# Kernel optimization log

Hardware: AMD Instinct MI355X
Metric: run time of the kernel (lower is better)

The kernel has to match this reference:

```python
import jax, jax.numpy as jnp
import numpy as np
import math

DIM = 128
HEADS = 8
HC = DIM // HEADS  # per-head channels = 16
N = 50000
E = 800000
LEAKY_SLOPE = 0.2


def _seg_softmax(logits, seg, n):
    # numerically-stable softmax over edges grouped by destination node
    m = jax.ops.segment_max(logits, seg, num_segments=n)
    m = jnp.where(jnp.isfinite(m), m, 0.0)
    e = jnp.exp(logits - m[seg])
    s = jax.ops.segment_sum(e, seg, num_segments=n)
    return e / jnp.maximum(s[seg], 1e-16)


def setup_inputs() -> dict:
    key = jax.random.key(0)
    ks = jax.random.split(key, 20)
    sc = 1.0 / math.sqrt(DIM)
    inp = {
        "x": jax.random.normal(ks[0], (N, DIM), jnp.float32),
        "edge_index": jax.random.randint(ks[1], (2, E), 0, N, jnp.int64),
        # GATConv params
        "gat_w": jax.random.normal(ks[2], (DIM, DIM), jnp.float32) * sc,
        "gat_att_src": jax.random.normal(ks[3], (HEADS, HC), jnp.float32) * sc,
        "gat_att_dst": jax.random.normal(ks[4], (HEADS, HC), jnp.float32) * sc,
        "gat_b": jnp.zeros((DIM,), jnp.float32),
        # SAGEConv params (lin_l has bias, lin_r has none; normalize=True)
        "sage_wl": jax.random.normal(ks[5], (DIM, DIM), jnp.float32) * sc,
        "sage_bl": jnp.zeros((DIM,), jnp.float32),
        "sage_wr": jax.random.normal(ks[6], (DIM, DIM), jnp.float32) * sc,
        # TransformerConv params (q/k/v + skip, heads concat -> DIM)
        "tr_wq": jax.random.normal(ks[7], (DIM, DIM), jnp.float32) * sc,
        "tr_bq": jnp.zeros((DIM,), jnp.float32),
        "tr_wk": jax.random.normal(ks[8], (DIM, DIM), jnp.float32) * sc,
        "tr_bk": jnp.zeros((DIM,), jnp.float32),
        "tr_wv": jax.random.normal(ks[9], (DIM, DIM), jnp.float32) * sc,
        "tr_bv": jnp.zeros((DIM,), jnp.float32),
        "tr_wskip": jax.random.normal(ks[10], (DIM, DIM), jnp.float32) * sc,
        "tr_bskip": jnp.zeros((DIM,), jnp.float32),
        # fusion + layernorm
        "fus_w": jax.random.normal(ks[11], (3 * DIM, DIM), jnp.float32) * (1.0 / math.sqrt(3 * DIM)),
        "fus_b": jnp.zeros((DIM,), jnp.float32),
        "ln_g": jnp.ones((DIM,), jnp.float32),
        "ln_b": jnp.zeros((DIM,), jnp.float32),
    }
    return inp


def reference(x, edge_index, gat_w, gat_att_src, gat_att_dst, gat_b,
              sage_wl, sage_bl, sage_wr,
              tr_wq, tr_bq, tr_wk, tr_bk, tr_wv, tr_bv, tr_wskip, tr_bskip,
              fus_w, fus_b, ln_g, ln_b):
    n = x.shape[0]
    src, dst = edge_index[0], edge_index[1]  # messages flow src -> dst

    # ---- GATConv (adds self-loops, per-dst softmax attention) ----
    loop = jnp.arange(n, dtype=src.dtype)
    s2 = jnp.concatenate([src, loop])
    d2 = jnp.concatenate([dst, loop])
    h = (x @ gat_w).reshape(n, HEADS, HC)            # [N,H,C]
    a_src = (h * gat_att_src).sum(-1)                # [N,H]
    a_dst = (h * gat_att_dst).sum(-1)
    logits = jax.nn.leaky_relu(a_src[s2] + a_dst[d2], LEAKY_SLOPE)  # [E+N,H]
    alpha = _seg_softmax(logits, d2, n)
    gat_out = jax.ops.segment_sum(alpha[:, :, None] * h[s2], d2,
                                  num_segments=n).reshape(n, DIM) + gat_b

    # ---- SAGEConv (mean aggregation + root weight, L2-normalized) ----
    ones = jnp.ones(src.shape, x.dtype)
    deg = jax.ops.segment_sum(ones, dst, num_segments=n)
    nbr = jax.ops.segment_sum(x[src], dst, num_segments=n) / jnp.maximum(deg, 1.0)[:, None]
    sage_out = nbr @ sage_wl + sage_bl + x @ sage_wr
    sage_out = sage_out / jnp.maximum(
        jnp.linalg.norm(sage_out, axis=-1, keepdims=True), 1e-12)

    # ---- TransformerConv (scaled dot-product attn per dst + skip) ----
    q = (x @ tr_wq + tr_bq).reshape(n, HEADS, HC)
    k = (x @ tr_wk + tr_bk).reshape(n, HEADS, HC)
    v = (x @ tr_wv + tr_bv).reshape(n, HEADS, HC)
    t_logits = (q[dst] * k[src]).sum(-1) / math.sqrt(HC)  # [E,H]
    t_alpha = _seg_softmax(t_logits, dst, n)               # dropout off (eval)
    tr_out = jax.ops.segment_sum(t_alpha[:, :, None] * v[src], dst,
                                 num_segments=n).reshape(n, DIM)
    tr_out = tr_out + x @ tr_wskip + tr_bskip

    # ---- fusion + layernorm ----
    concat = jnp.concatenate([gat_out, sage_out, tr_out], axis=-1)
    out = concat @ fus_w + fus_b
    mu = out.mean(-1, keepdims=True)
    var = ((out - mu) ** 2).mean(-1, keepdims=True)
    return (out - mu) / jnp.sqrt(var + 1e-5) * ln_g + ln_b
```

## Files before the change

### kernel.cpp

```cpp
#include <hip/hip_runtime.h>
#include <hip/hip_bf16.h>
#include <math.h>

#define DIM 128
#define HEADS 8

typedef short short8 __attribute__((ext_vector_type(8)));
typedef float f32x4 __attribute__((ext_vector_type(4)));

#define GLD_LDS16(g, l) \
  __builtin_amdgcn_global_load_lds((const __attribute__((address_space(1))) void*)(g), \
                                   (__attribute__((address_space(3))) void*)(l), 16, 0, 0)

__device__ __forceinline__ float bf2f(unsigned short u) {
  union { unsigned int i; float f; } c; c.i = ((unsigned int)u) << 16; return c.f;
}
__device__ __forceinline__ unsigned short f2bf(float f) {
  __hip_bfloat16 h = __float2bfloat16(f);
  union { __hip_bfloat16 h; unsigned short u; } c; c.h = h; return c.u;
}
__device__ __forceinline__ float u_lo(unsigned int u) {
  union { unsigned int i; float f; } c; c.i = u << 16; return c.f;
}
__device__ __forceinline__ float u_hi(unsigned int u) {
  union { unsigned int i; float f; } c; c.i = u & 0xffff0000u; return c.f;
}

__global__ void prep_w(const float* __restrict__ gw, const float* __restrict__ wq,
                       const float* __restrict__ wk, const float* __restrict__ wv,
                       const float* __restrict__ wsk,
                       const float* __restrict__ bq, const float* __restrict__ bk,
                       const float* __restrict__ bv, const float* __restrict__ bsk,
                       const float* __restrict__ swl, const float* __restrict__ swr,
                       const float* __restrict__ fw,
                       unsigned short* __restrict__ Wcat_t, float* __restrict__ Bcat,
                       unsigned short* __restrict__ sage_t, unsigned short* __restrict__ fus_t) {
  int i = blockIdx.x * 256 + threadIdx.x;
  if (i < 81920) {
    int c = i >> 7, k = i & 127;
    int s = c >> 7, j = c & 127;
    const float* w = (s == 0) ? gw : (s == 1) ? wq : (s == 2) ? wk : (s == 3) ? wv : wsk;
    Wcat_t[i] = f2bf(w[k * 128 + j]);
  } else if (i < 114688) {
    int t = i - 81920;
    int j = t >> 8, k = t & 255;
    float v = (k < 128) ? swl[k * 128 + j] : swr[(k - 128) * 128 + j];
    sage_t[t] = f2bf(v);
  } else if (i < 163840) {
    int t = i - 114688;
    int j = t / 384, k = t - j * 384;
    fus_t[t] = f2bf(fw[k * 128 + j]);
  } else if (i < 164480) {
    int c = i - 163840;
    int s = c >> 7, j = c & 127;
    Bcat[c] = (s == 0) ? 0.f : (s == 1) ? bq[j] : (s == 2) ? bk[j] : (s == 3) ? bv[j] : bsk[j];
  }
}

__global__ void convert_x(const float* __restrict__ x, unsigned short* __restrict__ AG, int n) {
  int i = blockIdx.x * 256 + threadIdx.x;
  if (i >= n * 32) return;
  int idx = i * 4;
  float4 v = *(const float4*)(x + idx);
  ushort4 u;
  u.x = f2bf(v.x); u.y = f2bf(v.y); u.z = f2bf(v.z); u.w = f2bf(v.w);
  *(ushort4*)(AG + (size_t)(idx >> 7) * 512 + 384 + (idx & 127)) = u;
}

template <int EPI>
__global__ __launch_bounds__(256) void gemm128(
    const __hip_bfloat16* __restrict__ A0, int lda0,
    const __hip_bfloat16* __restrict__ A1, int lda1,
    const __hip_bfloat16* __restrict__ Bt, int K,
    const float* __restrict__ bias,
    unsigned short* __restrict__ AGo, float* __restrict__ Pq, float* __restrict__ Psk,
    float* __restrict__ aSo, float* __restrict__ aDo,
    const float* __restrict__ atts, const float* __restrict__ attd,
    unsigned short* __restrict__ FUSo, float* __restrict__ outF,
    const float* __restrict__ lng, const float* __restrict__ lnb,
    int M) {
  __shared__ char Asb[128 * 64];
  __shared__ char Bsb[128 * 64];
  int tid = threadIdx.x;
  int l = tid & 63, w = tid >> 6;
  int row0 = blockIdx.x * 128, col0 = blockIdx.y * 128;
  f32x4 acc[2][8] = {};

  for (int kt = 0; kt < K; kt += 32) {
    const __hip_bfloat16* Ap;
    int lda, kof;
    if (A1 != nullptr && kt >= 128) { Ap = A1; lda = lda1; kof = kt - 128; }
    else { Ap = A0; lda = lda0; kof = kt; }
#pragma unroll
    for (int it = 0; it < 2; ++it) {
      int c = it * 256 + tid;
      int r = c >> 2, cp = c & 3;
      int gp = cp ^ (r & 3);
      int gr = row0 + r; if (gr >= M) gr = M - 1;
      GLD_LDS16((const char*)(Ap + (size_t)gr * lda + kof) + gp * 16, Asb + c * 16);
    }
#pragma unroll
    for (int it = 0; it < 2; ++it) {
      int c = it * 256 + tid;
      int r = c >> 2, cp = c & 3;
      int gp = cp ^ (r & 3);
      GLD_LDS16((const char*)(Bt + (size_t)(col0 + r) * K + kt) + gp * 16, Bsb + c * 16);
    }
    __syncthreads();
    int g = l >> 4, ri = l & 15;
    short8 af[2], bfr[8];
#pragma unroll
    for (int m = 0; m < 2; ++m) {
      int r = w * 32 + m * 16 + ri;
      af[m] = *(const short8*)(Asb + r * 64 + ((g ^ (r & 3)) * 16));
    }
#pragma unroll
    for (int c4 = 0; c4 < 8; ++c4) {
      int r = c4 * 16 + ri;
      bfr[c4] = *(const short8*)(Bsb + r * 64 + ((g ^ (r & 3)) * 16));
    }
#pragma unroll
    for (int m = 0; m < 2; ++m)
#pragma unroll
      for (int c4 = 0; c4 < 8; ++c4)
        acc[m][c4] = __builtin_amdgcn_mfma_f32_16x16x32_bf16(af[m], bfr[c4], acc[m][c4], 0, 0, 0);
    __syncthreads();
  }

  int g = l >> 4, ri = l & 15;
  float bias_r[8];
#pragma unroll
  for (int c4 = 0; c4 < 8; ++c4) bias_r[c4] = bias[col0 + c4 * 16 + ri];

  if (EPI == 0) {
    int y = col0 >> 7;
    if (y == 0) {
      float as_w[8], ad_w[8];
#pragma unroll
      for (int c4 = 0; c4 < 8; ++c4) { as_w[c4] = atts[c4 * 16 + ri]; ad_w[c4] = attd[c4 * 16 + ri]; }
#pragma unroll
      for (int m = 0; m < 2; ++m) {
#pragma unroll
        for (int j = 0; j < 4; ++j) {
          int row = row0 + w * 32 + m * 16 + g * 4 + j;
          bool ok = (row < M);
#pragma unroll
          for (int c4 = 0; c4 < 8; ++c4) {
            float v = acc[m][c4][j];
            if (ok) AGo[(size_t)row * 512 + c4 * 16 + ri] = f2bf(v);
            float p1 = v * as_w[c4], p2 = v * ad_w[c4];
            p1 += __shfl_xor(p1, 1); p1 += __shfl_xor(p1, 2);
            p1 += __shfl_xor(p1, 4); p1 += __shfl_xor(p1, 8);
            p2 += __shfl_xor(p2, 1); p2 += __shfl_xor(p2, 2);
            p2 += __shfl_xor(p2, 4); p2 += __shfl_xor(p2, 8);
            if (ok && ri == 0) { aSo[row * HEADS + c4] = p1; aDo[row * HEADS + c4] = p2; }
          }
        }
      }
    } else {
#pragma unroll
      for (int m = 0; m < 2; ++m) {
#pragma unroll
        for (int j = 0; j < 4; ++j) {
          int row = row0 + w * 32 + m * 16 + g * 4 + j;
          if (row >= M) continue;
#pragma unroll
          for (int c4 = 0; c4 < 8; ++c4) {
            int c = c4 * 16 + ri;
            float v = acc[m][c4][j] + bias_r[c4];
            if (y == 1)      Pq[(size_t)row * 128 + c] = v;
            else if (y == 2) AGo[(size_t)row * 512 + 128 + c] = f2bf(v);
            else if (y == 3) AGo[(size_t)row * 512 + 256 + c] = f2bf(v);
            else             Psk[(size_t)row * 128 + c] = v;
          }
        }
      }
    }
  } else {
#pragma unroll
    for (int m = 0; m < 2; ++m) {
#pragma unroll
      for (int j = 0; j < 4; ++j) {
        int row = row0 + w * 32 + m * 16 + g * 4 + j;
        bool ok = (row < M);
        float v[8];
        float s = 0.f;
#pragma unroll
        for (int c4 = 0; c4 < 8; ++c4) {
          v[c4] = acc[m][c4][j] + bias_r[c4];
          if (EPI == 1) s += v[c4] * v[c4];
          else          s += v[c4];
        }
        s += __shfl_xor(s, 1); s += __shfl_xor(s, 2);
        s += __shfl_xor(s, 4); s += __shfl_xor(s, 8);
        if (EPI == 1) {
          float inv = 1.f / fmaxf(sqrtf(s), 1e-12f);
          if (ok) {
#pragma unroll
            for (int c4 = 0; c4 < 8; ++c4)
              FUSo[(size_t)row * 384 + 128 + c4 * 16 + ri] = f2bf(v[c4] * inv);
          }
        } else {
          float mu = s * (1.f / 128.f);
          float ss = 0.f;
#pragma unroll
          for (int c4 = 0; c4 < 8; ++c4) { float d = v[c4] - mu; ss += d * d; }
          ss += __shfl_xor(ss, 1); ss += __shfl_xor(ss, 2);
          ss += __shfl_xor(ss, 4); ss += __shfl_xor(ss, 8);
          float rstd = 1.f / sqrtf(ss * (1.f / 128.f) + 1e-5f);
          if (ok) {
#pragma unroll
            for (int c4 = 0; c4 < 8; ++c4) {
              int c = c4 * 16 + ri;
              outF[(size_t)row * 128 + c] = (v[c4] - mu) * rstd * lng[c] + lnb[c];
            }
          }
        }
      }
    }
  }
}

__global__ void deg_hist(const int* __restrict__ ei, int* __restrict__ deg, int E) {
  int e = blockIdx.x * 256 + threadIdx.x;
  if (e < E) atomicAdd(&deg[ei[E + e]], 1);
}

__global__ void bsum_k(const int* __restrict__ deg, int* __restrict__ bsum, int n) {
  int blk = blockIdx.x, t = threadIdx.x;
  int base = blk * 1024 + t * 4;
  int s = 0;
  if (base + 3 < n) {
    int4 d = *(const int4*)(deg + base);
    s = d.x + d.y + d.z + d.w;
  } else {
#pragma unroll
    for (int j = 0; j < 4; ++j) { int i = base + j; if (i < n) s += deg[i]; }
  }
  int lane = t & 63, wid = t >> 6;
  int x = s;
#pragma unroll
  for (int d = 1; d < 64; d <<= 1) { int y = __shfl_up(x, d); if (lane >= d) x += y; }
  __shared__ int wsum[4];
  if (lane == 63) wsum[wid] = x;
  __syncthreads();
  if (t == 0) bsum[blk] = wsum[0] + wsum[1] + wsum[2] + wsum[3];
}

__global__ void bscan_k(const int* __restrict__ bsum, int* __restrict__ bpref,
                        int* __restrict__ total_out, int nb) {
  int lane = threadIdx.x;
  int carry = 0;
  for (int base = 0; base < nb; base += 64) {
    int i = base + lane;
    int v = (i < nb) ? bsum[i] : 0;
    int x = v;
#pragma unroll
    for (int d = 1; d < 64; d <<= 1) { int y = __shfl_up(x, d); if (lane >= d) x += y; }
    if (i < nb) bpref[i] = carry + x - v;
    carry += __shfl(x, 63);
  }
  if (lane == 0) total_out[0] = carry;
}

__global__ void offs_k(const int* __restrict__ deg, const int* __restrict__ bpref,
                       int* __restrict__ offs, int* __restrict__ cursor, int n) {
  int blk = blockIdx.x, t = threadIdx.x;
  int base = blk * 1024 + t * 4;
  int d0 = 0, d1 = 0, d2 = 0, d3 = 0;
  if (base + 3 < n) {
    int4 d = *(const int4*)(deg + base);
    d0 = d.x; d1 = d.y; d2 = d.z; d3 = d.w;
  } else {
    if (base + 0 < n) d0 = deg[base + 0];
    if (base + 1 < n) d1 = deg[base + 1];
    if (base + 2 < n) d2 = deg[base + 2];
    if (base + 3 < n) d3 = deg[base + 3];
  }
  int s = d0 + d1 + d2 + d3;
  int lane = t & 63, wid = t >> 6;
  int x = s;
#pragma unroll
  for (int d = 1; d < 64; d <<= 1) { int y = __shfl_up(x, d); if (lane >= d) x += y; }
  __shared__ int wsum[4];
  if (lane == 63) wsum[wid] = x;
  __syncthreads();
  int woff = 0;
  for (int ww = 0; ww < wid; ++ww) woff += wsum[ww];
  int excl = bpref[blk] + woff + x - s;
  int p0 = excl, p1 = excl + d0, p2 = p1 + d1, p3 = p2 + d2;
  if (base + 0 < n) { offs[base + 0] = p0; cursor[base + 0] = p0; }
  if (base + 1 < n) { offs[base + 1] = p1; cursor[base + 1] = p1; }
  if (base + 2 < n) { offs[base + 2] = p2; cursor[base + 2] = p2; }
  if (base + 3 < n) { offs[base + 3] = p3; cursor[base + 3] = p3; }
}

__global__ void scatter_k(const int* __restrict__ ei, int* __restrict__ cursor,
                          int* __restrict__ csrc, int E) {
  int e = blockIdx.x * 256 + threadIdx.x;
  if (e >= E) return;
  int src = ei[e], dst = ei[E + e];
  int pos = atomicAdd(&cursor[dst], 1);
  csrc[pos] = src;
}

__global__ __launch_bounds__(256) void aggregate(
    const unsigned short* __restrict__ AG, const float* __restrict__ Pq,
    const float* __restrict__ Psk,
    const float* __restrict__ aS, const float* __restrict__ aD,
    const int* __restrict__ offs, const int* __restrict__ csrc,
    const float* __restrict__ gat_b,
    unsigned short* __restrict__ FUS, unsigned short* __restrict__ nbrb, int n) {
  int node = blockIdx.x * 4 + (threadIdx.x >> 6);
  if (node >= n) return;
  int lane = threadIdx.x & 63;
  int head = lane >> 3;
  const unsigned short* An = AG + (size_t)node * 512;
  float2 qv = *(const float2*)(Pq + (size_t)node * 128 + 2 * lane);
  float adst = aD[node * HEADS + head];

  float lg0 = aS[node * HEADS + head] + adst;
  lg0 = fmaxf(lg0, 0.2f * lg0);
  float m_g = lg0, l_g = 1.f;
  unsigned int hu0 = *(const unsigned int*)(An + 2 * lane);
  float2 acc_g = { u_lo(hu0), u_hi(hu0) };

  float m_t = -1e30f, l_t = 0.f;
  float2 acc_t = {0.f, 0.f};
  float2 acc_s = {0.f, 0.f};

  int e0 = offs[node], e1 = offs[node + 1];

#define EDGE_UPDATE(HU, KU, VU, XU, AV)                                  \
  {                                                                      \
    float lg = (AV) + adst;                                              \
    lg = fmaxf(lg, 0.2f * lg);                                           \
    float mg = fmaxf(m_g, lg);                                           \
    float scg = __expf(m_g - mg), wg = __expf(lg - mg);                  \
    acc_g.x = acc_g.x * scg + wg * u_lo(HU);                             \
    acc_g.y = acc_g.y * scg + wg * u_hi(HU);                             \
    l_g = l_g * scg + wg; m_g = mg;                                      \
    float part = qv.x * u_lo(KU) + qv.y * u_hi(KU);                      \
    part += __shfl_xor(part, 1);                                         \
    part += __shfl_xor(part, 2);                                         \
    part += __shfl_xor(part, 4);                                         \
    float tl = part * 0.25f;                                             \
    float mt = fmaxf(m_t, tl);                                           \
    float sct = __expf(m_t - mt), wt = __expf(tl - mt);                  \
    acc_t.x = acc_t.x * sct + wt * u_lo(VU);                             \
    acc_t.y = acc_t.y * sct + wt * u_hi(VU);                             \
    l_t = l_t * sct + wt; m_t = mt;                                      \
    acc_s.x += u_lo(XU);                                                 \
    acc_s.y += u_hi(XU);                                                 \
  }

#define LOAD_EDGE(u, si_a, hu_a, ku_a, vu_a, xu_a, av_a)                 \
  {                                                                      \
    const unsigned short* As = AG + (size_t)si_a[u] * 512;               \
    hu_a[u] = *(const unsigned int*)(As + 2 * lane);                     \
    ku_a[u] = *(const unsigned int*)(As + 128 + 2 * lane);               \
    vu_a[u] = *(const unsigned int*)(As + 256 + 2 * lane);               \
    xu_a[u] = *(const unsigned int*)(As + 384 + 2 * lane);               \
    av_a[u] = aS[si_a[u] * HEADS + head];                                \
  }

  int e = e0;
  for (; e + 8 <= e1; e += 8) {
    int si[8];
#pragma unroll
    for (int u = 0; u < 8; ++u) si[u] = csrc[e + u];
    unsigned int hu[8], ku[8], vu[8], xu[8];
    float av[8];
#pragma unroll
    for (int u = 0; u < 8; ++u) LOAD_EDGE(u, si, hu, ku, vu, xu, av);
#pragma unroll
    for (int u = 0; u < 8; ++u) EDGE_UPDATE(hu[u], ku[u], vu[u], xu[u], av[u]);
  }
  if (e + 4 <= e1) {
    int si[4];
#pragma unroll
    for (int u = 0; u < 4; ++u) si[u] = csrc[e + u];
    unsigned int hu[4], ku[4], vu[4], xu[4];
    float av[4];
#pragma unroll
    for (int u = 0; u < 4; ++u) LOAD_EDGE(u, si, hu, ku, vu, xu, av);
#pragma unroll
    for (int u = 0; u < 4; ++u) EDGE_UPDATE(hu[u], ku[u], vu[u], xu[u], av[u]);
    e += 4;
  }
  for (; e < e1; ++e) {
    int s = csrc[e];
    const unsigned short* As = AG + (size_t)s * 512;
    unsigned int hu = *(const unsigned int*)(As + 2 * lane);
    unsigned int ku = *(const unsigned int*)(As + 128 + 2 * lane);
    unsigned int vu = *(const unsigned int*)(As + 256 + 2 * lane);
    unsigned int xu = *(const unsigned int*)(As + 384 + 2 * lane);
    float av = aS[s * HEADS + head];
    EDGE_UPDATE(hu, ku, vu, xu, av);
  }
#undef EDGE_UPDATE
#undef LOAD_EDGE

  float gx = acc_g.x / l_g + gat_b[2 * lane];
  float gy = acc_g.y / l_g + gat_b[2 * lane + 1];
  ushort2 go = { f2bf(gx), f2bf(gy) };
  *(ushort2*)(FUS + (size_t)node * 384 + 2 * lane) = go;

  float2 skip = *(const float2*)(Psk + (size_t)node * 128 + 2 * lane);
  float tx, ty;
  if (l_t > 0.f) {
    tx = acc_t.x / l_t + skip.x;
    ty = acc_t.y / l_t + skip.y;
  } else { tx = skip.x; ty = skip.y; }
  ushort2 to = { f2bf(tx), f2bf(ty) };
  *(ushort2*)(FUS + (size_t)node * 384 + 256 + 2 * lane) = to;

  float dg = fmaxf((float)(e1 - e0), 1.f);
  float inv = 1.f / dg;
  ushort2 nb = { f2bf(acc_s.x * inv), f2bf(acc_s.y * inv) };
  *(ushort2*)(nbrb + (size_t)node * 128 + 2 * lane) = nb;
}

extern "C" void kernel_launch(void* const* d_in, const int* in_sizes, int n_in,
                              void* d_out, int out_size, void* d_ws, size_t ws_size,
                              hipStream_t stream) {
  const float* x      = (const float*)d_in[0];
  const int*   ei     = (const int*)d_in[1];
  const float* gat_w  = (const float*)d_in[2];
  const float* att_s  = (const float*)d_in[3];
  const float* att_d  = (const float*)d_in[4];
  const float* gat_b  = (const float*)d_in[5];
  const float* swl    = (const float*)d_in[6];
  const float* sbl    = (const float*)d_in[7];
  const float* swr    = (const float*)d_in[8];
  const float* wq     = (const float*)d_in[9];
  const float* bq     = (const float*)d_in[10];
  const float* wk     = (const float*)d_in[11];
  const float* bk     = (const float*)d_in[12];
  const float* wv     = (const float*)d_in[13];
  const float* bv     = (const float*)d_in[14];
  const float* wsk    = (const float*)d_in[15];
  const float* bsk    = (const float*)d_in[16];
  const float* fus_w  = (const float*)d_in[17];
  const float* fus_b  = (const float*)d_in[18];
  const float* ln_g   = (const float*)d_in[19];
  const float* ln_b   = (const float*)d_in[20];
  float* out = (float*)d_out;

  const int n = in_sizes[0] / DIM;
  const int E = in_sizes[1] / 2;

  char* wsb = (char*)d_ws;
  size_t o = 0;
  auto carve = [&](size_t bytes) { char* p = wsb + o; o += (bytes + 255) & ~(size_t)255; return p; };
  unsigned short* Wcat_t = (unsigned short*)carve(640 * 128 * 2);
  float*          Bcat   = (float*)carve(640 * 4);
  unsigned short* sage_t = (unsigned short*)carve(128 * 256 * 2);
  unsigned short* fus_t  = (unsigned short*)carve(128 * 384 * 2);
  unsigned short* AG     = (unsigned short*)carve((size_t)n * 512 * 2);
  float*          Pqs    = (float*)carve((size_t)n * 128 * 4);
  float*          Psk    = (float*)carve((size_t)n * 128 * 4);
  float*          aS     = (float*)carve((size_t)n * HEADS * 4);
  float*          aD     = (float*)carve((size_t)n * HEADS * 4);
  unsigned short* FUS    = (unsigned short*)carve((size_t)n * 384 * 2);
  unsigned short* nbrb   = (unsigned short*)carve((size_t)n * 128 * 2);
  int* ideg   = (int*)carve((size_t)n * 4);
  int* offs   = (int*)carve(((size_t)n + 1) * 4);
  int* cursor = (int*)carve((size_t)n * 4);
  int* csrc   = (int*)carve((size_t)E * 4);
  const int NB = (n + 1023) / 1024;
  int* bsum   = (int*)carve((size_t)NB * 4);
  int* bpref  = (int*)carve((size_t)NB * 4);

  hipMemsetAsync(ideg, 0, n * sizeof(int), stream);

  prep_w<<<(164480 + 255) / 256, 256, 0, stream>>>(
      gat_w, wq, wk, wv, wsk, bq, bk, bv, bsk, swl, swr, fus_w,
      Wcat_t, Bcat, sage_t, fus_t);
  convert_x<<<(n * 32 + 255) / 256, 256, 0, stream>>>(x, AG, n);

  const int RB = (n + 127) / 128;

  gemm128<0><<<dim3(RB, 5), 256, 0, stream>>>(
      (const __hip_bfloat16*)(AG + 384), 512, nullptr, 0,
      (const __hip_bfloat16*)Wcat_t, 128, Bcat,
      AG, Pqs, Psk, aS, aD, att_s, att_d, nullptr, nullptr, nullptr, nullptr, n);

  deg_hist<<<(E + 255) / 256, 256, 0, stream>>>(ei, ideg, E);
  bsum_k<<<NB, 256, 0, stream>>>(ideg, bsum, n);
  bscan_k<<<1, 64, 0, stream>>>(bsum, bpref, offs + n, NB);
  offs_k<<<NB, 256, 0, stream>>>(ideg, bpref, offs, cursor, n);
  scatter_k<<<(E + 255) / 256, 256, 0, stream>>>(ei, cursor, csrc, E);

  aggregate<<<(n + 3) / 4, 256, 0, stream>>>(AG, Pqs, Psk, aS, aD, offs, csrc,
                                             gat_b, FUS, nbrb, n);

  gemm128<1><<<dim3(RB, 1), 256, 0, stream>>>(
      (const __hip_bfloat16*)nbrb, 128, (const __hip_bfloat16*)(AG + 384), 512,
      (const __hip_bfloat16*)sage_t, 256, sbl,
      nullptr, nullptr, nullptr, nullptr, nullptr, nullptr, nullptr,
      FUS, nullptr, nullptr, nullptr, n);

  gemm128<2><<<dim3(RB, 1), 256, 0, stream>>>(
      (const __hip_bfloat16*)FUS, 384, nullptr, 0,
      (const __hip_bfloat16*)fus_t, 384, fus_b,
      nullptr, nullptr, nullptr, nullptr, nullptr, nullptr, nullptr,
      nullptr, out, ln_g, ln_b, n);
}
```

Measured before the change: 422.1 us.

## Fold GAT attention projections into GEMM and drop online-softmax max tracking

Precomputes W·att_src and W·att_dst as an extra 128-column block of the concatenated weight matrix, so the per-head attention scalars come straight out of the GEMM instead of from shuffle reductions in the epilogue. The aggregation kernel replaces online softmax (running max plus rescaling) with a plain exp-and-sum, which removes two exps and several multiplies per edge. The cost is an extra GEMM column tile that is mostly zero work, bf16 rounding of the folded attention weights, and a risk of exp overflow because the max subtraction is gone.

Result: no change. 419.2 us (-0.7%).

```diff
diff --git a/kernel.cpp b/kernel.cpp
--- a/kernel.cpp
+++ b/kernel.cpp
@@ -31,29 +31,49 @@
                        const float* __restrict__ wsk,
                        const float* __restrict__ bq, const float* __restrict__ bk,
                        const float* __restrict__ bv, const float* __restrict__ bsk,
+                       const float* __restrict__ atts, const float* __restrict__ attd,
                        const float* __restrict__ swl, const float* __restrict__ swr,
                        const float* __restrict__ fw,
                        unsigned short* __restrict__ Wcat_t, float* __restrict__ Bcat,
                        unsigned short* __restrict__ sage_t, unsigned short* __restrict__ fus_t) {
   int i = blockIdx.x * 256 + threadIdx.x;
-  if (i < 81920) {
+  if (i < 98304) {
     int c = i >> 7, k = i & 127;
     int s = c >> 7, j = c & 127;
-    const float* w = (s == 0) ? gw : (s == 1) ? wq : (s == 2) ? wk : (s == 3) ? wv : wsk;
-    Wcat_t[i] = f2bf(w[k * 128 + j]);
-  } else if (i < 114688) {
-    int t = i - 81920;
+    float val;
+    if (s <= 4) {
+      const float* w = (s == 0) ? gw : (s == 1) ? wq : (s == 2) ? wk : (s == 3) ? wv : wsk;
+      val = w[k * 128 + j];
+    } else {
+      if (j < 8) {
+        float acc = 0.f;
+#pragma unroll
+        for (int t = 0; t < 16; ++t) acc += gw[k * 128 + j * 16 + t] * atts[j * 16 + t];
+        val = acc;
+      } else if (j < 16) {
+        int h = j - 8;
+        float acc = 0.f;
+#pragma unroll
+        for (int t = 0; t < 16; ++t) acc += gw[k * 128 + h * 16 + t] * attd[h * 16 + t];
+        val = acc;
+      } else {
+        val = 0.f;
+      }
+    }
+    Wcat_t[i] = f2bf(val);
+  } else if (i < 131072) {
+    int t = i - 98304;
     int j = t >> 8, k = t & 255;
     float v = (k < 128) ? swl[k * 128 + j] : swr[(k - 128) * 128 + j];
     sage_t[t] = f2bf(v);
-  } else if (i < 163840) {
-    int t = i - 114688;
+  } else if (i < 180224) {
+    int t = i - 131072;
     int j = t / 384, k = t - j * 384;
     fus_t[t] = f2bf(fw[k * 128 + j]);
-  } else if (i < 164480) {
-    int c = i - 163840;
+  } else if (i < 180992) {
+    int c = i - 180224;
     int s = c >> 7, j = c & 127;
-    Bcat[c] = (s == 0) ? 0.f : (s == 1) ? bq[j] : (s == 2) ? bk[j] : (s == 3) ? bv[j] : bsk[j];
+    Bcat[c] = (s == 1) ? bq[j] : (s == 2) ? bk[j] : (s == 3) ? bv[j] : (s == 4) ? bsk[j] : 0.f;
   }
 }
 
@@ -75,7 +95,6 @@
     const float* __restrict__ bias,
     unsigned short* __restrict__ AGo, float* __restrict__ Pq, float* __restrict__ Psk,
     float* __restrict__ aSo, float* __restrict__ aDo,
-    const float* __restrict__ atts, const float* __restrict__ attd,
     unsigned short* __restrict__ FUSo, float* __restrict__ outF,
     const float* __restrict__ lng, const float* __restrict__ lnb,
     int M) {
@@ -134,27 +153,16 @@
 
   if (EPI == 0) {
     int y = col0 >> 7;
-    if (y == 0) {
-      float as_w[8], ad_w[8];
-#pragma unroll
-      for (int c4 = 0; c4 < 8; ++c4) { as_w[c4] = atts[c4 * 16 + ri]; ad_w[c4] = attd[c4 * 16 + ri]; }
+    if (y == 5) {
 #pragma unroll
       for (int m = 0; m < 2; ++m) {
 #pragma unroll
         for (int j = 0; j < 4; ++j) {
           int row = row0 + w * 32 + m * 16 + g * 4 + j;
-          bool ok = (row < M);
-#pragma unroll
-          for (int c4 = 0; c4 < 8; ++c4) {
-            float v = acc[m][c4][j];
-            if (ok) AGo[(size_t)row * 512 + c4 * 16 + ri] = f2bf(v);
-            float p1 = v * as_w[c4], p2 = v * ad_w[c4];
-            p1 += __shfl_xor(p1, 1); p1 += __shfl_xor(p1, 2);
-            p1 += __shfl_xor(p1, 4); p1 += __shfl_xor(p1, 8);
-            p2 += __shfl_xor(p2, 1); p2 += __shfl_xor(p2, 2);
-            p2 += __shfl_xor(p2, 4); p2 += __shfl_xor(p2, 8);
-            if (ok && ri == 0) { aSo[row * HEADS + c4] = p1; aDo[row * HEADS + c4] = p2; }
-          }
+          if (row >= M) continue;
+          float v = acc[m][0][j];
+          if (ri < 8) aSo[row * HEADS + ri] = v;
+          else        aDo[row * HEADS + (ri - 8)] = v;
         }
       }
     } else {
@@ -168,7 +176,8 @@
           for (int c4 = 0; c4 < 8; ++c4) {
             int c = c4 * 16 + ri;
             float v = acc[m][c4][j] + bias_r[c4];
-            if (y == 1)      Pq[(size_t)row * 128 + c] = v;
+            if (y == 0)      AGo[(size_t)row * 512 + c] = f2bf(v);
+            else if (y == 1) Pq[(size_t)row * 128 + c] = v;
             else if (y == 2) AGo[(size_t)row * 512 + 128 + c] = f2bf(v);
             else if (y == 3) AGo[(size_t)row * 512 + 256 + c] = f2bf(v);
             else             Psk[(size_t)row * 128 + c] = v;
@@ -315,17 +324,18 @@
   if (node >= n) return;
   int lane = threadIdx.x & 63;
   int head = lane >> 3;
-  const unsigned short* An = AG + (size_t)node * 512;
   float2 qv = *(const float2*)(Pq + (size_t)node * 128 + 2 * lane);
   float adst = aD[node * HEADS + head];
 
   float lg0 = aS[node * HEADS + head] + adst;
   lg0 = fmaxf(lg0, 0.2f * lg0);
-  float m_g = lg0, l_g = 1.f;
-  unsigned int hu0 = *(const unsigned int*)(An + 2 * lane);
-  float2 acc_g = { u_lo(hu0), u_hi(hu0) };
-
-  float m_t = -1e30f, l_t = 0.f;
+  float w0 = __expf(lg0);
+  const char* Anb = (const char*)AG + ((size_t)node << 10) + lane * 4;
+  unsigned int hu0 = *(const unsigned int*)(Anb);
+  float2 acc_g = { w0 * u_lo(hu0), w0 * u_hi(hu0) };
+  float l_g = w0;
+
+  float l_t = 0.f;
   float2 acc_t = {0.f, 0.f};
   float2 acc_s = {0.f, 0.f};
 
@@ -335,32 +345,29 @@
   {                                                                      \
     float lg = (AV) + adst;                                              \
     lg = fmaxf(lg, 0.2f * lg);                                           \
-    float mg = fmaxf(m_g, lg);                                           \
-    float scg = __expf(m_g - mg), wg = __expf(lg - mg);                  \
-    acc_g.x = acc_g.x * scg + wg * u_lo(HU);                             \
-    acc_g.y = acc_g.y * scg + wg * u_hi(HU);                             \
-    l_g = l_g * scg + wg; m_g = mg;                                      \
+    float wg = __expf(lg);                                               \
+    acc_g.x += wg * u_lo(HU);                                            \
+    acc_g.y += wg * u_hi(HU);                                            \
+    l_g += wg;                                                           \
     float part = qv.x * u_lo(KU) + qv.y * u_hi(KU);                      \
     part += __shfl_xor(part, 1);                                         \
     part += __shfl_xor(part, 2);                                         \
     part += __shfl_xor(part, 4);                                         \
-    float tl = part * 0.25f;                                             \
-    float mt = fmaxf(m_t, tl);                                           \
-    float sct = __expf(m_t - mt), wt = __expf(tl - mt);                  \
-    acc_t.x = acc_t.x * sct + wt * u_lo(VU);                             \
-    acc_t.y = acc_t.y * sct + wt * u_hi(VU);                             \
-    l_t = l_t * sct + wt; m_t = mt;                                      \
+    float wt = __expf(part * 0.25f);                                     \
+    acc_t.x += wt * u_lo(VU);                                            \
+    acc_t.y += wt * u_hi(VU);                                            \
+    l_t += wt;                                                           \
     acc_s.x += u_lo(XU);                                                 \
     acc_s.y += u_hi(XU);                                                 \
   }
 
 #define LOAD_EDGE(u, si_a, hu_a, ku_a, vu_a, xu_a, av_a)                 \
   {                                                                      \
-    const unsigned short* As = AG + (size_t)si_a[u] * 512;               \
-    hu_a[u] = *(const unsigned int*)(As + 2 * lane);                     \
-    ku_a[u] = *(const unsigned int*)(As + 128 + 2 * lane);               \
-    vu_a[u] = *(const unsigned int*)(As + 256 + 2 * lane);               \
-    xu_a[u] = *(const unsigned int*)(As + 384 + 2 * lane);               \
+    const char* As = (const char*)AG + ((size_t)si_a[u] << 10) + lane * 4; \
+    hu_a[u] = *(const unsigned int*)(As);                                \
+    ku_a[u] = *(const unsigned int*)(As + 256);                          \
+    vu_a[u] = *(const unsigned int*)(As + 512);                          \
+    xu_a[u] = *(const unsigned int*)(As + 768);                          \
     av_a[u] = aS[si_a[u] * HEADS + head];                                \
   }
 
@@ -390,11 +397,11 @@
   }
   for (; e < e1; ++e) {
     int s = csrc[e];
-    const unsigned short* As = AG + (size_t)s * 512;
-    unsigned int hu = *(const unsigned int*)(As + 2 * lane);
-    unsigned int ku = *(const unsigned int*)(As + 128 + 2 * lane);
-    unsigned int vu = *(const unsigned int*)(As + 256 + 2 * lane);
-    unsigned int xu = *(const unsigned int*)(As + 384 + 2 * lane);
+    const char* As = (const char*)AG + ((size_t)s << 10) + lane * 4;
+    unsigned int hu = *(const unsigned int*)(As);
+    unsigned int ku = *(const unsigned int*)(As + 256);
+    unsigned int vu = *(const unsigned int*)(As + 512);
+    unsigned int xu = *(const unsigned int*)(As + 768);
     float av = aS[s * HEADS + head];
     EDGE_UPDATE(hu, ku, vu, xu, av);
   }
@@ -453,8 +460,8 @@
   char* wsb = (char*)d_ws;
   size_t o = 0;
   auto carve = [&](size_t bytes) { char* p = wsb + o; o += (bytes + 255) & ~(size_t)255; return p; };
-  unsigned short* Wcat_t = (unsigned short*)carve(640 * 128 * 2);
-  float*          Bcat   = (float*)carve(640 * 4);
+  unsigned short* Wcat_t = (unsigned short*)carve(768 * 128 * 2);
+  float*          Bcat   = (float*)carve(768 * 4);
   unsigned short* sage_t = (unsigned short*)carve(128 * 256 * 2);
   unsigned short* fus_t  = (unsigned short*)carve(128 * 384 * 2);
   unsigned short* AG     = (unsigned short*)carve((size_t)n * 512 * 2);
@@ -474,17 +481,17 @@
 
   hipMemsetAsync(ideg, 0, n * sizeof(int), stream);
 
-  prep_w<<<(164480 + 255) / 256, 256, 0, stream>>>(
-      gat_w, wq, wk, wv, wsk, bq, bk, bv, bsk, swl, swr, fus_w,
+  prep_w<<<(180992 + 255) / 256, 256, 0, stream>>>(
+      gat_w, wq, wk, wv, wsk, bq, bk, bv, bsk, att_s, att_d, swl, swr, fus_w,
       Wcat_t, Bcat, sage_t, fus_t);
   convert_x<<<(n * 32 + 255) / 256, 256, 0, stream>>>(x, AG, n);
 
   const int RB = (n + 127) / 128;
 
-  gemm128<0><<<dim3(RB, 5), 256, 0, stream>>>(
+  gemm128<0><<<dim3(RB, 6), 256, 0, stream>>>(
       (const __hip_bfloat16*)(AG + 384), 512, nullptr, 0,
       (const __hip_bfloat16*)Wcat_t, 128, Bcat,
-      AG, Pqs, Psk, aS, aD, att_s, att_d, nullptr, nullptr, nullptr, nullptr, n);
+      AG, Pqs, Psk, aS, aD, nullptr, nullptr, nullptr, nullptr, n);
 
   deg_hist<<<(E + 255) / 256, 256, 0, stream>>>(ei, ideg, E);
   bsum_k<<<NB, 256, 0, stream>>>(ideg, bsum, n);
@@ -498,12 +505,12 @@
   gemm128<1><<<dim3(RB, 1), 256, 0, stream>>>(
       (const __hip_bfloat16*)nbrb, 128, (const __hip_bfloat16*)(AG + 384), 512,
       (const __hip_bfloat16*)sage_t, 256, sbl,
-      nullptr, nullptr, nullptr, nullptr, nullptr, nullptr, nullptr,
+      nullptr, nullptr, nullptr, nullptr, nullptr,
       FUS, nullptr, nullptr, nullptr, n);
 
   gemm128<2><<<dim3(RB, 1), 256, 0, stream>>>(
       (const __hip_bfloat16*)FUS, 384, nullptr, 0,
       (const __hip_bfloat16*)fus_t, 384, fus_b,
-      nullptr, nullptr, nullptr, nullptr, nullptr, nullptr, nullptr,
+      nullptr, nullptr, nullptr, nullptr, nullptr,
       nullptr, out, ln_g, ln_b, n);
 }
```
